# Kernel optimization log

Measured on AMD Instinct MI355X. Metric: run time of the kernel, lower is better.

The kernel has to match this reference:

```python
import jax, jax.numpy as jnp
import numpy as np

HIDDEN = 768
HEADS = 12
HEAD_DIM = HIDDEN // HEADS
DEPTH = 8
B, S = 4, 512


def setup_inputs() -> dict:
    key = jax.random.key(0)
    ks = jax.random.split(key, 12)
    sc = 0.02
    return {
        "hidden_states": jax.random.normal(ks[0], (B, S, HIDDEN), dtype=jnp.float32),
        "attention_mask": jnp.ones((B, S), dtype=jnp.int32),
        "Wq": jax.random.normal(ks[1], (HIDDEN, HIDDEN), dtype=jnp.float32) * sc,
        "bq": jnp.zeros((HIDDEN,), dtype=jnp.float32),
        "Wk": jax.random.normal(ks[2], (HIDDEN, HIDDEN), dtype=jnp.float32) * sc,
        "bk": jnp.zeros((HIDDEN,), dtype=jnp.float32),
        "Wv": jax.random.normal(ks[3], (HIDDEN, HIDDEN), dtype=jnp.float32) * sc,
        "bv": jnp.zeros((HIDDEN,), dtype=jnp.float32),
        "Wqd": jax.random.normal(ks[4], (HIDDEN * DEPTH, HIDDEN), dtype=jnp.float32) * sc,
        "bqd": jnp.zeros((HIDDEN * DEPTH,), dtype=jnp.float32),
        "Wkd": jax.random.normal(ks[5], (HIDDEN * DEPTH, HIDDEN), dtype=jnp.float32) * sc,
        "bkd": jnp.zeros((HIDDEN * DEPTH,), dtype=jnp.float32),
    }


def reference(hidden_states, attention_mask, Wq, bq, Wk, bk, Wv, bv, Wqd, bqd, Wkd, bkd):
    b, s, _ = hidden_states.shape
    # projections (nn.Linear: x @ W.T + b)
    V = (hidden_states @ Wv.T + bv).reshape(b, s, HEADS, HEAD_DIM).transpose(0, 2, 1, 3)  # [B,H,S,hd]
    Qd = (hidden_states @ Wqd.T + bqd).reshape(b, s, HEADS, HEAD_DIM, DEPTH).transpose(0, 2, 1, 3, 4)  # [B,H,S,hd,D]
    Kd = (hidden_states @ Wkd.T + bkd).reshape(b, s, HEADS, HEAD_DIM, DEPTH).transpose(0, 2, 1, 3, 4)
    # per-depth QK^T scores: [B,H,Sq,Sk,D]
    scores = jnp.einsum('bhqed,bhked->bhqkd', Qd, Kd) / np.sqrt(HEAD_DIM).astype(np.float32)
    # mask broadcasts over the key axis: [B,1,1,S,1]
    mask = attention_mask[:, None, None, :, None]
    scores = jnp.where(mask == 0, jnp.float32(-1e9), scores)
    # softmax over key dim (axis=-2 of [B,H,Sq,Sk,D])
    weights = jax.nn.softmax(scores, axis=3)
    # per-depth AV matmul, stacked on leading depth axis: [D,B,H,S,hd]
    depth_outputs = jnp.einsum('bhqkd,bhke->dbhqe', weights, V)
    return depth_outputs
```

## Files before the change

kernel.cpp:

```cpp
#include <hip/hip_runtime.h>

#define HIDDEN 768
#define HEADS 12
#define HEAD_DIM 64
#define DEPTH 8
#define BB 4
#define SS 512
#define MM (BB * SS)
#define NQD (HIDDEN * DEPTH)

typedef __bf16 bf16x8 __attribute__((ext_vector_type(8)));
typedef float f32x4 __attribute__((ext_vector_type(4)));
typedef float f32x16 __attribute__((ext_vector_type(16)));
typedef unsigned short u16x8 __attribute__((ext_vector_type(8)));

static __device__ __forceinline__ unsigned short f2bf(float f) {
  union { float f; unsigned u; } c; c.f = f;
  unsigned u = c.u;
  u = u + 0x7fffu + ((u >> 16) & 1u);
  return (unsigned short)(u >> 16);
}

static __device__ __forceinline__ unsigned cvt_pk_bf16(float lo, float hi) {
  unsigned r;
  asm("v_cvt_pk_bf16_f32 %0, %1, %2" : "=v"(r) : "v"(lo), "v"(hi));
  return r;
}

static __device__ __forceinline__ void gld16(const void* g, void* l) {
  __builtin_amdgcn_global_load_lds((const __attribute__((address_space(1))) void*)g,
                                   (__attribute__((address_space(3))) void*)l, 16, 0, 0);
}

__global__ void convert2_f32_bf16(const float* __restrict__ s0, unsigned short* __restrict__ d0,
                                  int n4_0, const float* __restrict__ s1,
                                  unsigned short* __restrict__ d1, int n4_1) {
  int i = blockIdx.x * blockDim.x + threadIdx.x;
  const float* src; unsigned short* dst; int j;
  if (i < n4_0) { src = s0; dst = d0; j = i; }
  else { j = i - n4_0; if (j >= n4_1) return; src = s1; dst = d1; }
  float4 v = reinterpret_cast<const float4*>(src)[j];
  ushort4 o;
  o.x = f2bf(v.x); o.y = f2bf(v.y); o.z = f2bf(v.z); o.w = f2bf(v.w);
  reinterpret_cast<ushort4*>(dst)[j] = o;
}

__global__ void convert_w_perm2(const float* __restrict__ s0, const float* __restrict__ s1,
                                unsigned short* __restrict__ dst, int n4each) {
  int i = blockIdx.x * blockDim.x + threadIdx.x;
  const float* src = s0; unsigned short* d = dst; int j = i;
  if (i >= n4each) {
    j = i - n4each;
    if (j >= n4each) return;
    src = s1; d = dst + (size_t)NQD * HIDDEN;
  }
  int row = j / 192;
  int cg  = j - row * 192;
  int nr = (row & ~511) | ((row & 7) << 6) | ((row >> 3) & 63);
  float4 v = reinterpret_cast<const float4*>(src)[j];
  ushort4 o;
  o.x = f2bf(v.x); o.y = f2bf(v.y); o.z = f2bf(v.z); o.w = f2bf(v.w);
  reinterpret_cast<ushort4*>(&d[(size_t)nr * HIDDEN])[cg] = o;
}

__global__ void convert_bias_perm2(const float* __restrict__ s0, const float* __restrict__ s1,
                                   float* __restrict__ dst, int n) {
  int i = blockIdx.x * blockDim.x + threadIdx.x;
  const float* src = s0; float* d = dst; int j = i;
  if (i >= n) {
    j = i - n;
    if (j >= n) return;
    src = s1; d = dst + n;
  }
  int nr = (j & ~511) | ((j & 7) << 6) | ((j >> 3) & 63);
  d[nr] = src[j];
}

__global__ __launch_bounds__(256) void gemm_bt(
    const unsigned short* __restrict__ A, const unsigned short* __restrict__ W,
    const float* __restrict__ bias, unsigned short* __restrict__ out0, int K) {
  __shared__ unsigned short At[2][4096];
  __shared__ unsigned short Bt[2][4096];
  const int tid = threadIdx.x;
  const int nwg = gridDim.x * gridDim.y;
  const int orig = blockIdx.y * gridDim.x + blockIdx.x;
  const int wg = (orig & 7) * (nwg >> 3) + (orig >> 3);
  const int bm = (wg % gridDim.x) * 128;
  const int bn = (wg / gridDim.x) * 128;
  const int wave = tid >> 6, lane = tid & 63;
  const int wm = (wave >> 1) * 64, wn = (wave & 1) * 64;
  const int lg = lane >> 4, lr = lane & 15;
  const int srow = tid >> 2, scol = (tid & 3) * 8;
  f32x4 acc[4][4] = {};
  const unsigned short* aptr = A + (size_t)(bm + srow) * K + scol;
  const unsigned short* wptr = W + (size_t)(bn + srow) * K + scol;

  auto stage = [&](int buf, int k0) {
    gld16(aptr + k0,                  &At[buf][tid * 8]);
    gld16(aptr + (size_t)64 * K + k0, &At[buf][2048 + tid * 8]);
    gld16(wptr + k0,                  &Bt[buf][tid * 8]);
    gld16(wptr + (size_t)64 * K + k0, &Bt[buf][2048 + tid * 8]);
  };

  stage(0, 0);
  __syncthreads();

  int cur = 0;
  for (int k0 = 32; k0 <= K; k0 += 32) {
    if (k0 < K) stage(cur ^ 1, k0);
    bf16x8 af[4], bfr[4];
#pragma unroll
    for (int mi = 0; mi < 4; ++mi)
      af[mi] = *reinterpret_cast<const bf16x8*>(&At[cur][(wm + mi * 16 + lr) * 32 + lg * 8]);
#pragma unroll
    for (int ni = 0; ni < 4; ++ni)
      bfr[ni] = *reinterpret_cast<const bf16x8*>(&Bt[cur][(wn + ni * 16 + lr) * 32 + lg * 8]);
#pragma unroll
    for (int mi = 0; mi < 4; ++mi)
#pragma unroll
      for (int ni = 0; ni < 4; ++ni)
        acc[mi][ni] = __builtin_amdgcn_mfma_f32_16x16x32_bf16(af[mi], bfr[ni], acc[mi][ni], 0, 0, 0);
    __syncthreads();
    cur ^= 1;
  }

#pragma unroll
  for (int mi = 0; mi < 4; ++mi)
#pragma unroll
    for (int ni = 0; ni < 4; ++ni)
#pragma unroll
      for (int i = 0; i < 4; ++i) {
        int m = bm + wm + mi * 16 + lg * 4 + i;
        int n = bn + wn + ni * 16 + lr;
        float v = acc[mi][ni][i] + bias[m];
        size_t addr = ((size_t)((n >> 9) * 12 + (m >> 6)) * 64 + (size_t)(m & 63)) * 512 + (size_t)(n & 511);
        out0[addr] = f2bf(v);
      }
}

__global__ __launch_bounds__(512, 2) void gemm_qk256(
    const unsigned short* __restrict__ A, const unsigned short* __restrict__ W,
    const float* __restrict__ bias, unsigned short* __restrict__ out0,
    unsigned short* __restrict__ out1, int K) {
  __shared__ unsigned short At[2][8192];
  __shared__ unsigned short Bt[2][6144];
  const int tid = threadIdx.x;
  const int nwg = gridDim.x * gridDim.y;
  const int orig = blockIdx.y * gridDim.x + blockIdx.x;
  const int wg = (orig & 7) * (nwg >> 3) + (orig >> 3);
  const int bm = (wg % gridDim.x) * 256;
  const int bn = (wg / gridDim.x) * 192;
  const int wave = tid >> 6, lane = tid & 63;
  const int wr = wave >> 2, wc = wave & 3;
  const int lg = lane >> 4, lr = lane & 15;

  const int tr = tid >> 2;
  const int cb = (tid & 3) * 16;
  const int colel = (cb ^ (((tr >> 1) & 3) << 4)) >> 1;
  const unsigned short* srcA = A + (size_t)(bm + tr) * K + colel;
  const unsigned short* srcW = W + (size_t)(bn + tr) * K + colel;

  f32x4 acc[8][3] = {};

  auto stage = [&](int buf, int k0) {
    gld16(srcA + k0,                   &At[buf][tid * 8]);
    gld16(srcA + (size_t)128 * K + k0, &At[buf][4096 + tid * 8]);
    gld16(srcW + k0,                   &Bt[buf][tid * 8]);
    if (tid < 256)
      gld16(srcW + (size_t)128 * K + k0, &Bt[buf][4096 + tid * 8]);
  };

  stage(0, 0);
  __syncthreads();

  const int rdswz = ((((lr >> 1) & 3) ^ lg) << 4);

  int cur = 0;
  for (int k0 = 32; k0 <= K; k0 += 32) {
    if (k0 < K) stage(cur ^ 1, k0);
    bf16x8 af[8], bfr[3];
    const char* abase = (const char*)&At[cur][0];
    const char* bbase = (const char*)&Bt[cur][0];
#pragma unroll
    for (int mi = 0; mi < 8; ++mi) {
      const int row = wr * 128 + mi * 16 + lr;
      af[mi] = *reinterpret_cast<const bf16x8*>(abase + row * 64 + rdswz);
    }
#pragma unroll
    for (int ni = 0; ni < 3; ++ni) {
      const int row = wc * 48 + ni * 16 + lr;
      bfr[ni] = *reinterpret_cast<const bf16x8*>(bbase + row * 64 + rdswz);
    }
#pragma unroll
    for (int mi = 0; mi < 8; ++mi)
#pragma unroll
      for (int ni = 0; ni < 3; ++ni)
        acc[mi][ni] = __builtin_amdgcn_mfma_f32_16x16x32_bf16(af[mi], bfr[ni], acc[mi][ni], 0, 0, 0);
    __syncthreads();
    cur ^= 1;
  }

  unsigned short* outp = out0;
  int nbase = 0;
  float scale = 0.125f;
  if (bn >= NQD) { outp = out1; nbase = NQD; scale = 1.0f; }
#pragma unroll
  for (int mi = 0; mi < 8; ++mi)
#pragma unroll
    for (int ni = 0; ni < 3; ++ni)
#pragma unroll
      for (int i = 0; i < 4; ++i) {
        int m = bm + wr * 128 + mi * 16 + lg * 4 + i;
        int n = bn + wc * 48 + ni * 16 + lr;
        float v = (acc[mi][ni][i] + bias[n]) * scale;
        int nr = n - nbase;
        size_t addr = ((size_t)(((m >> 9) * 12 + (nr >> 9)) * 8 + ((nr >> 6) & 7)) * 512 + (size_t)(m & 511)) * 64 + (size_t)(nr & 63);
        outp[addr] = f2bf(v);
      }
}

__global__ __launch_bounds__(256) void attn32(
    const unsigned short* __restrict__ Qd, const unsigned short* __restrict__ Kd,
    const unsigned short* __restrict__ Vt, const int* __restrict__ mask,
    float* __restrict__ out) {
  __shared__ unsigned char KsB[64 * 128];
  __shared__ unsigned char VsB[64 * 128];
  __shared__ float mLds[64];
  __shared__ int mflag;
  const int tid = threadIdx.x;
  const int bid = blockIdx.x;
  const int qt = bid & 3;
  const int inst = bid >> 2;
  const int bh = inst >> 3;
  const int b = bh / 12;
  const int wave = tid >> 6, lane = tid & 63;
  const int l31 = lane & 31, hi = lane >> 5;
  const size_t qkbase = (size_t)inst * (SS * 64);
  const size_t vbase = (size_t)bh * (64 * SS);

  if (tid == 0) mflag = 0;
  __syncthreads();
  {
    int m0 = mask[b * SS + tid], m1 = mask[b * SS + 256 + tid];
    if ((m0 == 0) || (m1 == 0)) mflag = 1;
  }
  __syncthreads();
  const bool hasmask = (mflag != 0);

  const int q0w = qt * 128 + wave * 32;
  bf16x8 aq[4];
  {
    const unsigned short* qrow = Qd + qkbase + (size_t)(q0w + l31) * 64 + 8 * hi;
#pragma unroll
    for (int s = 0; s < 4; ++s)
      aq[s] = *reinterpret_cast<const bf16x8*>(qrow + 16 * s);
  }

  const int sr = tid >> 3;
  const int sc = (tid & 7) * 8;
  const int swz_lo = sr * 128 + ((sc * 2) ^ ((sr & 7) << 4));
  const int swz_hi = (sr + 32) * 128 + ((sc * 2) ^ (((sr + 32) & 7) << 4));

  f32x16 o[2] = {};
  float psum = 0.f;

  u16x8 rk0 = *reinterpret_cast<const u16x8*>(&Kd[qkbase + (size_t)sr * 64 + sc]);
  u16x8 rk1 = *reinterpret_cast<const u16x8*>(&Kd[qkbase + (size_t)(sr + 32) * 64 + sc]);
  u16x8 rv0 = *reinterpret_cast<const u16x8*>(&Vt[vbase + (size_t)sr * SS + sc]);
  u16x8 rv1 = *reinterpret_cast<const u16x8*>(&Vt[vbase + (size_t)(sr + 32) * SS + sc]);

  for (int t = 0; t < SS / 64; ++t) {
    *reinterpret_cast<u16x8*>(KsB + swz_lo) = rk0;
    *reinterpret_cast<u16x8*>(KsB + swz_hi) = rk1;
    *reinterpret_cast<u16x8*>(VsB + swz_lo) = rv0;
    *reinterpret_cast<u16x8*>(VsB + swz_hi) = rv1;
    if (hasmask && tid < 64) mLds[tid] = mask[b * SS + t * 64 + tid] ? 0.f : -1e9f;
    __syncthreads();

    if (t < SS / 64 - 1) {
      const int kn = (t + 1) * 64;
      rk0 = *reinterpret_cast<const u16x8*>(&Kd[qkbase + (size_t)(kn + sr) * 64 + sc]);
      rk1 = *reinterpret_cast<const u16x8*>(&Kd[qkbase + (size_t)(kn + sr + 32) * 64 + sc]);
      rv0 = *reinterpret_cast<const u16x8*>(&Vt[vbase + (size_t)sr * SS + kn + sc]);
      rv1 = *reinterpret_cast<const u16x8*>(&Vt[vbase + (size_t)(sr + 32) * SS + kn + sc]);
    }

    f32x16 st[2];
#pragma unroll
    for (int kh = 0; kh < 2; ++kh) {
      f32x16 acc = {};
      const int row = kh * 32 + l31;
      const int rswz = (row & 7) << 4;
#pragma unroll
      for (int s = 0; s < 4; ++s) {
        bf16x8 ak = *reinterpret_cast<const bf16x8*>(KsB + row * 128 + ((32 * s + 16 * hi) ^ rswz));
        acc = __builtin_amdgcn_mfma_f32_32x32x16_bf16(ak, aq[s], acc, 0, 0, 0);
      }
      st[kh] = acc;
    }

    if (hasmask) {
#pragma unroll
      for (int h = 0; h < 2; ++h)
#pragma unroll
        for (int r = 0; r < 16; ++r)
          st[h][r] += mLds[32 * h + (r & 3) + 8 * (r >> 2) + 4 * hi];
    }

    float pv[2][16];
#pragma unroll
    for (int h = 0; h < 2; ++h)
#pragma unroll
      for (int r = 0; r < 16; ++r) {
        float p = __expf(st[h][r]);
        psum += p;
        pv[h][r] = p;
      }

#pragma unroll
    for (int ks = 0; ks < 4; ++ks) {
      const int h = ks >> 1, rb = 8 * (ks & 1);
      unsigned w0 = cvt_pk_bf16(pv[h][rb + 0], pv[h][rb + 1]);
      unsigned w1 = cvt_pk_bf16(pv[h][rb + 2], pv[h][rb + 3]);
      unsigned w2 = cvt_pk_bf16(pv[h][rb + 4], pv[h][rb + 5]);
      unsigned w3 = cvt_pk_bf16(pv[h][rb + 6], pv[h][rb + 7]);
      asm("v_permlane32_swap_b32 %0, %1" : "+v"(w0), "+v"(w2));
      asm("v_permlane32_swap_b32 %0, %1" : "+v"(w1), "+v"(w3));
      union { unsigned u[4]; bf16x8 v; } pa;
      pa.u[0] = w0; pa.u[1] = w1; pa.u[2] = w2; pa.u[3] = w3;
#pragma unroll
      for (int et = 0; et < 2; ++et) {
        const int vrow = 32 * et + l31;
        bf16x8 bv = *reinterpret_cast<const bf16x8*>(
            VsB + vrow * 128 + ((32 * ks + 16 * hi) ^ ((vrow & 7) << 4)));
        o[et] = __builtin_amdgcn_mfma_f32_32x32x16_bf16(pa.v, bv, o[et], 0, 0, 0);
      }
    }
    __syncthreads();
  }

  psum += __shfl_xor(psum, 32);
  float inv = 1.f / psum;
  float iv[16];
#pragma unroll
  for (int r = 0; r < 16; ++r)
    iv[r] = __shfl(inv, (r & 3) + 8 * (r >> 2) + 4 * hi);

  const int d = inst & 7;
  const int hh = bh % 12;
  const size_t obase = (((size_t)d * BB + b) * HEADS + hh) * (SS * 64);
#pragma unroll
  for (int et = 0; et < 2; ++et)
#pragma unroll
    for (int r = 0; r < 16; ++r) {
      const int qrow = (r & 3) + 8 * (r >> 2) + 4 * hi;
      out[obase + (size_t)(q0w + qrow) * 64 + 32 * et + l31] = o[et][r] * iv[r];
    }
}

extern "C" void kernel_launch(void* const* d_in, const int* in_sizes, int n_in,
                              void* d_out, int out_size, void* d_ws, size_t ws_size,
                              hipStream_t stream) {
  const float* hs  = (const float*)d_in[0];
  const int* mask  = (const int*)d_in[1];
  const float* Wv  = (const float*)d_in[6];
  const float* bv  = (const float*)d_in[7];
  const float* Wqd = (const float*)d_in[8];
  const float* bqd = (const float*)d_in[9];
  const float* Wkd = (const float*)d_in[10];
  const float* bkd = (const float*)d_in[11];

  char* ws = (char*)d_ws;
  unsigned short* A_bf   = (unsigned short*)ws; ws += (size_t)MM * HIDDEN * 2;
  unsigned short* Wv_bf  = (unsigned short*)ws; ws += (size_t)HIDDEN * HIDDEN * 2;
  unsigned short* Wqk_bf = (unsigned short*)ws; ws += (size_t)(2 * NQD) * HIDDEN * 2;
  float*          bqk_p  = (float*)ws;          ws += (size_t)(2 * NQD) * 4;
  unsigned short* Qd     = (unsigned short*)ws; ws += (size_t)MM * NQD * 2;
  unsigned short* Kd     = (unsigned short*)ws; ws += (size_t)MM * NQD * 2;
  unsigned short* Vt     = (unsigned short*)ws; ws += (size_t)MM * HIDDEN * 2;

  {
    int a4 = MM * HIDDEN / 4, b4 = HIDDEN * HIDDEN / 4;
    convert2_f32_bf16<<<(a4 + b4 + 255) / 256, 256, 0, stream>>>(hs, A_bf, a4, Wv, Wv_bf, b4);
  }
  {
    int n4 = NQD * HIDDEN / 4;
    convert_w_perm2<<<(2 * n4 + 255) / 256, 256, 0, stream>>>(Wqd, Wkd, Wqk_bf, n4);
    convert_bias_perm2<<<(2 * NQD + 255) / 256, 256, 0, stream>>>(bqd, bkd, bqk_p, NQD);
  }

  gemm_bt<<<dim3(HIDDEN / 128, MM / 128), 256, 0, stream>>>(
      Wv_bf, A_bf, bv, Vt, HIDDEN);
  gemm_qk256<<<dim3(MM / 256, 2 * NQD / 192), 512, 0, stream>>>(
      A_bf, Wqk_bf, bqk_p, Qd, Kd, HIDDEN);

  attn32<<<BB * HEADS * DEPTH * (SS / 128), 256, 0, stream>>>(Qd, Kd, Vt, mask, (float*)d_out);
}
```

Baseline: 139.4 us.

## Replace direct global-to-LDS loads with register-staged double-buffered prefetch in QK GEMM

The QK projection GEMM previously used direct global-to-LDS loads (gld16) into a double buffer. It now loads tiles into registers two k-steps ahead, using two register sets, and writes them to LDS after the MFMA compute on the current buffer. The aim is to hide global memory latency behind compute with a deeper prefetch. The cost is extra VGPRs for the staging registers under launch_bounds(512,2), plus separate LDS store instructions.

Measured after the change: 132.1 us. 1.06x faster.

```diff
diff --git a/kernel.cpp b/kernel.cpp
--- a/kernel.cpp
+++ b/kernel.cpp
@@ -154,33 +154,54 @@
   const int wr = wave >> 2, wc = wave & 3;
   const int lg = lane >> 4, lr = lane & 15;
 
-  const int tr = tid >> 2;
-  const int cb = (tid & 3) * 16;
-  const int colel = (cb ^ (((tr >> 1) & 3) << 4)) >> 1;
-  const unsigned short* srcA = A + (size_t)(bm + tr) * K + colel;
-  const unsigned short* srcW = W + (size_t)(bn + tr) * K + colel;
+  const int rA0 = tid >> 2,           cA0 = (tid & 3) << 3;
+  const int rA1 = (tid + 512) >> 2;
+  const bool hasB1 = tid < 256;
+  const int rB1 = (tid + 512) >> 2;
+  const int dA0 = rA0 * 64 + ((cA0 << 1) ^ (((rA0 >> 1) & 3) << 4));
+  const int dA1 = rA1 * 64 + ((cA0 << 1) ^ (((rA1 >> 1) & 3) << 4));
+  const int dB0 = dA0;
+  const int dB1 = rB1 * 64 + ((cA0 << 1) ^ (((rB1 >> 1) & 3) << 4));
+  const unsigned short* pA0 = A + (size_t)(bm + rA0) * K + cA0;
+  const unsigned short* pA1 = A + (size_t)(bm + rA1) * K + cA0;
+  const unsigned short* pB0 = W + (size_t)(bn + rA0) * K + cA0;
+  const unsigned short* pB1 = W + (size_t)(bn + rB1) * K + cA0;
+
+  u16x8 a0A = {}, a1A = {}, b0A = {}, b1A = {};
+  u16x8 a0B = {}, a1B = {}, b0B = {}, b1B = {};
+
+  auto gloadA = [&](int k0) {
+    a0A = *reinterpret_cast<const u16x8*>(pA0 + k0);
+    a1A = *reinterpret_cast<const u16x8*>(pA1 + k0);
+    b0A = *reinterpret_cast<const u16x8*>(pB0 + k0);
+    if (hasB1) b1A = *reinterpret_cast<const u16x8*>(pB1 + k0);
+  };
+  auto gloadB = [&](int k0) {
+    a0B = *reinterpret_cast<const u16x8*>(pA0 + k0);
+    a1B = *reinterpret_cast<const u16x8*>(pA1 + k0);
+    b0B = *reinterpret_cast<const u16x8*>(pB0 + k0);
+    if (hasB1) b1B = *reinterpret_cast<const u16x8*>(pB1 + k0);
+  };
+  auto lwriteA = [&](int buf) {
+    *reinterpret_cast<u16x8*>((char*)At[buf] + dA0) = a0A;
+    *reinterpret_cast<u16x8*>((char*)At[buf] + dA1) = a1A;
+    *reinterpret_cast<u16x8*>((char*)Bt[buf] + dB0) = b0A;
+    if (hasB1) *reinterpret_cast<u16x8*>((char*)Bt[buf] + dB1) = b1A;
+  };
+  auto lwriteB = [&](int buf) {
+    *reinterpret_cast<u16x8*>((char*)At[buf] + dA0) = a0B;
+    *reinterpret_cast<u16x8*>((char*)At[buf] + dA1) = a1B;
+    *reinterpret_cast<u16x8*>((char*)Bt[buf] + dB0) = b0B;
+    if (hasB1) *reinterpret_cast<u16x8*>((char*)Bt[buf] + dB1) = b1B;
+  };
+
+  const int rdswz = ((((lr >> 1) & 3) ^ lg) << 4);
 
   f32x4 acc[8][3] = {};
-
-  auto stage = [&](int buf, int k0) {
-    gld16(srcA + k0,                   &At[buf][tid * 8]);
-    gld16(srcA + (size_t)128 * K + k0, &At[buf][4096 + tid * 8]);
-    gld16(srcW + k0,                   &Bt[buf][tid * 8]);
-    if (tid < 256)
-      gld16(srcW + (size_t)128 * K + k0, &Bt[buf][4096 + tid * 8]);
-  };
-
-  stage(0, 0);
-  __syncthreads();
-
-  const int rdswz = ((((lr >> 1) & 3) ^ lg) << 4);
-
-  int cur = 0;
-  for (int k0 = 32; k0 <= K; k0 += 32) {
-    if (k0 < K) stage(cur ^ 1, k0);
+  auto compute = [&](int buf) {
     bf16x8 af[8], bfr[3];
-    const char* abase = (const char*)&At[cur][0];
-    const char* bbase = (const char*)&Bt[cur][0];
+    const char* abase = (const char*)At[buf];
+    const char* bbase = (const char*)Bt[buf];
 #pragma unroll
     for (int mi = 0; mi < 8; ++mi) {
       const int row = wr * 128 + mi * 16 + lr;
@@ -196,8 +217,25 @@
 #pragma unroll
       for (int ni = 0; ni < 3; ++ni)
         acc[mi][ni] = __builtin_amdgcn_mfma_f32_16x16x32_bf16(af[mi], bfr[ni], acc[mi][ni], 0, 0, 0);
+  };
+
+  const int NT = K / 32;
+  gloadA(0);
+  gloadB(32);
+  lwriteA(0);
+  __syncthreads();
+
+  for (int tt = 0; tt < NT; tt += 2) {
+    if (tt + 2 < NT) gloadA((tt + 2) * 32);
+    compute(0);
+    if (tt + 1 < NT) lwriteB(1);
     __syncthreads();
-    cur ^= 1;
+    if (tt + 1 < NT) {
+      if (tt + 3 < NT) gloadB((tt + 3) * 32);
+      compute(1);
+      if (tt + 2 < NT) lwriteA(0);
+      __syncthreads();
+    }
   }
 
   unsigned short* outp = out0;
```

## Deepen QK projection GEMM K-tile to 64 with explicit waitcnt scheduling and setprio

Applied to the files above, without the earlier changes.

Reworks the Qd/Kd projection GEMM mainloop to stage K=64 tiles (128-byte rows with XOR swizzle) instead of K=32. It also interleaves A-fragment LDS reads with MFMA groups, using manual s_waitcnt, sched_barrier and s_barrier in place of __syncthreads. s_setprio is raised around the MFMA sections in both the GEMM and the attention kernel to favour matrix issue across waves. The aim is fewer barriers per K and better overlap of global loads with compute, at the cost of doubled LDS use, which may reduce occupancy.

Measured after the change: 136.5 us. -2.1%, faster.

```diff
diff --git a/kernel.cpp b/kernel.cpp
--- a/kernel.cpp
+++ b/kernel.cpp
@@ -142,8 +142,8 @@
     const unsigned short* __restrict__ A, const unsigned short* __restrict__ W,
     const float* __restrict__ bias, unsigned short* __restrict__ out0,
     unsigned short* __restrict__ out1, int K) {
-  __shared__ unsigned short At[2][8192];
-  __shared__ unsigned short Bt[2][6144];
+  __shared__ unsigned short At[2][256 * 64];
+  __shared__ unsigned short Bt[2][192 * 64];
   const int tid = threadIdx.x;
   const int nwg = gridDim.x * gridDim.y;
   const int orig = blockIdx.y * gridDim.x + blockIdx.x;
@@ -154,50 +154,68 @@
   const int wr = wave >> 2, wc = wave & 3;
   const int lg = lane >> 4, lr = lane & 15;
 
-  const int tr = tid >> 2;
-  const int cb = (tid & 3) * 16;
-  const int colel = (cb ^ (((tr >> 1) & 3) << 4)) >> 1;
-  const unsigned short* srcA = A + (size_t)(bm + tr) * K + colel;
-  const unsigned short* srcW = W + (size_t)(bn + tr) * K + colel;
+  const int srow = tid >> 3;
+  const int scol = 8 * ((tid & 7) ^ ((tid >> 3) & 7));
+  const unsigned short* pA = A + (size_t)(bm + srow) * K + scol;
+  const unsigned short* pB = W + (size_t)(bn + srow) * K + scol;
+
+  auto stage = [&](int buf, int k0) {
+#pragma unroll
+    for (int j = 0; j < 4; ++j)
+      gld16(pA + (size_t)(j * 64) * K + k0, (char*)At[buf] + j * 8192 + tid * 16);
+#pragma unroll
+    for (int j = 0; j < 3; ++j)
+      gld16(pB + (size_t)(j * 64) * K + k0, (char*)Bt[buf] + j * 8192 + tid * 16);
+  };
+
+  const int rdx = (lr & 7) << 4;
 
   f32x4 acc[8][3] = {};
 
-  auto stage = [&](int buf, int k0) {
-    gld16(srcA + k0,                   &At[buf][tid * 8]);
-    gld16(srcA + (size_t)128 * K + k0, &At[buf][4096 + tid * 8]);
-    gld16(srcW + k0,                   &Bt[buf][tid * 8]);
-    if (tid < 256)
-      gld16(srcW + (size_t)128 * K + k0, &Bt[buf][4096 + tid * 8]);
-  };
-
   stage(0, 0);
-  __syncthreads();
-
-  const int rdswz = ((((lr >> 1) & 3) ^ lg) << 4);
-
-  int cur = 0;
-  for (int k0 = 32; k0 <= K; k0 += 32) {
-    if (k0 < K) stage(cur ^ 1, k0);
-    bf16x8 af[8], bfr[3];
-    const char* abase = (const char*)&At[cur][0];
-    const char* bbase = (const char*)&Bt[cur][0];
-#pragma unroll
-    for (int mi = 0; mi < 8; ++mi) {
-      const int row = wr * 128 + mi * 16 + lr;
-      af[mi] = *reinterpret_cast<const bf16x8*>(abase + row * 64 + rdswz);
-    }
+  asm volatile("s_waitcnt vmcnt(0)" ::: "memory");
+  __builtin_amdgcn_sched_barrier(0);
+  __builtin_amdgcn_s_barrier();
+
+  int c = 0;
+  const int NT = K / 64;
+  for (int t = 0; t < NT; ++t) {
+    const char* ab = (const char*)At[c];
+    const char* bb = (const char*)Bt[c];
+    if (t + 1 < NT) stage(c ^ 1, (t + 1) * 64);
+    bf16x8 bfr[3][2];
 #pragma unroll
     for (int ni = 0; ni < 3; ++ni) {
       const int row = wc * 48 + ni * 16 + lr;
-      bfr[ni] = *reinterpret_cast<const bf16x8*>(bbase + row * 64 + rdswz);
-    }
-#pragma unroll
-    for (int mi = 0; mi < 8; ++mi)
-#pragma unroll
-      for (int ni = 0; ni < 3; ++ni)
-        acc[mi][ni] = __builtin_amdgcn_mfma_f32_16x16x32_bf16(af[mi], bfr[ni], acc[mi][ni], 0, 0, 0);
-    __syncthreads();
-    cur ^= 1;
+      bfr[ni][0] = *reinterpret_cast<const bf16x8*>(bb + row * 128 + ((lg * 16) ^ rdx));
+      bfr[ni][1] = *reinterpret_cast<const bf16x8*>(bb + row * 128 + ((64 + lg * 16) ^ rdx));
+    }
+#pragma unroll
+    for (int p = 0; p < 4; ++p) {
+      const int m0 = wr * 128 + (2 * p) * 16 + lr;
+      const int m1 = m0 + 16;
+      bf16x8 a00 = *reinterpret_cast<const bf16x8*>(ab + m0 * 128 + ((lg * 16) ^ rdx));
+      bf16x8 a01 = *reinterpret_cast<const bf16x8*>(ab + m0 * 128 + ((64 + lg * 16) ^ rdx));
+      bf16x8 a10 = *reinterpret_cast<const bf16x8*>(ab + m1 * 128 + ((lg * 16) ^ rdx));
+      bf16x8 a11 = *reinterpret_cast<const bf16x8*>(ab + m1 * 128 + ((64 + lg * 16) ^ rdx));
+      asm volatile("s_waitcnt lgkmcnt(0)" ::: "memory");
+      __builtin_amdgcn_sched_barrier(0);
+      __builtin_amdgcn_s_setprio(1);
+#pragma unroll
+      for (int ni = 0; ni < 3; ++ni) {
+        acc[2 * p][ni]     = __builtin_amdgcn_mfma_f32_16x16x32_bf16(a00, bfr[ni][0], acc[2 * p][ni], 0, 0, 0);
+        acc[2 * p][ni]     = __builtin_amdgcn_mfma_f32_16x16x32_bf16(a01, bfr[ni][1], acc[2 * p][ni], 0, 0, 0);
+        acc[2 * p + 1][ni] = __builtin_amdgcn_mfma_f32_16x16x32_bf16(a10, bfr[ni][0], acc[2 * p + 1][ni], 0, 0, 0);
+        acc[2 * p + 1][ni] = __builtin_amdgcn_mfma_f32_16x16x32_bf16(a11, bfr[ni][1], acc[2 * p + 1][ni], 0, 0, 0);
+      }
+      __builtin_amdgcn_s_setprio(0);
+      if (p == 3) {
+        asm volatile("s_waitcnt vmcnt(0)" ::: "memory");
+        __builtin_amdgcn_sched_barrier(0);
+      }
+      __builtin_amdgcn_s_barrier();
+    }
+    c ^= 1;
   }
 
   unsigned short* outp = out0;
@@ -286,6 +304,7 @@
     }
 
     f32x16 st[2];
+    __builtin_amdgcn_s_setprio(1);
 #pragma unroll
     for (int kh = 0; kh < 2; ++kh) {
       f32x16 acc = {};
@@ -298,6 +317,7 @@
       }
       st[kh] = acc;
     }
+    __builtin_amdgcn_s_setprio(0);
 
     if (hasmask) {
 #pragma unroll
@@ -317,6 +337,7 @@
         pv[h][r] = p;
       }
 
+    __builtin_amdgcn_s_setprio(1);
 #pragma unroll
     for (int ks = 0; ks < 4; ++ks) {
       const int h = ks >> 1, rb = 8 * (ks & 1);
@@ -336,6 +357,7 @@
         o[et] = __builtin_amdgcn_mfma_f32_32x32x16_bf16(pa.v, bv, o[et], 0, 0, 0);
       }
     }
+    __builtin_amdgcn_s_setprio(0);
     __syncthreads();
   }
 
```
